# Performance work log

Hardware: AMD Instinct MI355X
Metric: run time of the kernel (lower is better)

## Reference

```python
import jax, jax.numpy as jnp
import numpy as np
import math

H = 8
D_MODEL = 512
D_K = D_MODEL // H
NEG = -1.0e9


def setup_inputs() -> dict:
    key = jax.random.key(0)
    ks = jax.random.split(key, 10)
    B, S, D = 8, 1024, D_MODEL
    s = 1.0 / math.sqrt(D)
    return {
        "query": jax.random.normal(ks[0], (B, S, D), jnp.float32),
        "key": jax.random.normal(ks[1], (B, S, D), jnp.float32),
        "value": jax.random.normal(ks[2], (B, S, D), jnp.float32),
        "group_prob": jax.random.uniform(ks[3], (B, S, S), jnp.float32),
        "Wq": jax.random.normal(ks[4], (D, D), jnp.float32) * s,
        "Wk": jax.random.normal(ks[5], (D, D), jnp.float32) * s,
        "Wv": jax.random.normal(ks[6], (D, D), jnp.float32) * s,
        "Wh": jax.random.normal(ks[7], (D, D), jnp.float32) * s,
        "bh": jax.random.normal(ks[8], (D,), jnp.float32) * s,
        "mask": jax.random.randint(ks[9], (B, S, S), 0, 2, jnp.int32),
    }


def reference(query, key, value, group_prob, Wq, Wk, Wv, Wh, bh, mask):
    B, S, D = query.shape
    # project and split heads: [B, H, S, d_k]
    def split(x, W):
        return (x @ W.T).reshape(B, S, H, D_K).transpose(0, 2, 1, 3)
    q, k, v = split(query, Wq), split(key, Wk), split(value, Wv)
    scores = jnp.einsum('bhqd,bhkd->bhqk', q, k) / jnp.sqrt(jnp.asarray(D_K, q.dtype))
    # masked_fill where (mask | eye) == 0, i.e. keep mask-allowed or diagonal positions
    eye = jnp.eye(S, dtype=jnp.int32)
    allowed = (mask[:, None, :, :] | eye[None, None, :, :]) != 0  # [B,1,S,S]
    scores = jnp.where(allowed, scores, jnp.asarray(NEG, scores.dtype))
    p_attn = jax.nn.softmax(scores, axis=-1)
    p_attn = p_attn * group_prob[:, None, :, :]  # post-softmax group scaling
    x = jnp.einsum('bhqk,bhkd->bhqd', p_attn, v)
    x = x.transpose(0, 2, 1, 3).reshape(B, S, D)
    return x @ Wh.T + bh
```

## Files before the change

kernel.cpp:

```cpp
#include <hip/hip_runtime.h>
#include <hip/hip_bf16.h>
#include <cstdint>


typedef __attribute__((ext_vector_type(8))) short short8;
typedef __attribute__((ext_vector_type(4))) float f32x4;

__device__ __forceinline__ ushort f2bf(float x) {
    union { __hip_bfloat16 h; ushort u; } v;
    v.h = __float2bfloat16(x);
    return v.u;
}
__device__ __forceinline__ float bf2f(ushort u) {
    union { uint u; float f; } v; v.u = ((uint)u) << 16; return v.f;
}
__device__ __forceinline__ f32x4 mfma16(short8 a, short8 b, f32x4 c) {
    return __builtin_amdgcn_mfma_f32_16x16x32_bf16(a, b, c, 0, 0, 0);
}

__global__ __launch_bounds__(256)
void gm_prep(const int* __restrict__ mask, const float* __restrict__ gp,
             ushort* __restrict__ gm)
{
    size_t i = ((size_t)blockIdx.x * 256 + threadIdx.x) * 4;
    int4 m = *(const int4*)(mask + i);
    float4 g = *(const float4*)(gp + i);
    int k = (int)(i & 1023), q = (int)((i >> 10) & 1023);
    const ushort neg = f2bf(-1.0f);
    ushort4 o;
    o.x = (m.x != 0 || q == k + 0) ? f2bf(g.x) : neg;
    o.y = (m.y != 0 || q == k + 1) ? f2bf(g.y) : neg;
    o.z = (m.z != 0 || q == k + 2) ? f2bf(g.z) : neg;
    o.w = (m.w != 0 || q == k + 3) ? f2bf(g.w) : neg;
    *(ushort4*)(gm + i) = o;
}

__global__ __launch_bounds__(256)
void qkv_gemm(const float* __restrict__ Xq, const float* __restrict__ Xk,
              const float* __restrict__ Xv,
              const float* __restrict__ Wq, const float* __restrict__ Wk,
              const float* __restrict__ Wv,
              ushort* __restrict__ q_ws, ushort* __restrict__ k_ws,
              ushort* __restrict__ vT)
{
    __shared__ __attribute__((aligned(16))) ushort As[128][40];
    __shared__ __attribute__((aligned(16))) ushort Bs[128][40];

    const int z = blockIdx.z;
    const float* A  = (z == 0) ? Xq : (z == 1) ? Xk : Wv;
    const float* Bm = (z == 0) ? Wq : (z == 1) ? Wk : Xv;
    const int mt = (z == 2) ? blockIdx.y : blockIdx.x;
    const int nt = (z == 2) ? blockIdx.x : blockIdx.y;
    const int m0 = mt * 128, n0 = nt * 128;
    const int tid = threadIdx.x;
    const int lane = tid & 63, wave = tid >> 6;
    const int l15 = lane & 15, g = lane >> 4;
    const int wm = wave >> 1, wn = wave & 1;
    const int srow = tid >> 1, skh = (tid & 1) * 16;

    f32x4 acc[4][4];
    #pragma unroll
    for (int i = 0; i < 4; ++i)
        #pragma unroll
        for (int j = 0; j < 4; ++j) acc[i][j] = (f32x4){0.f, 0.f, 0.f, 0.f};

    const float* Arow = A  + (size_t)(m0 + srow) * 512 + skh;
    const float* Brow = Bm + (size_t)(n0 + srow) * 512 + skh;

    for (int k0 = 0; k0 < 512; k0 += 32) {
        {
            float4 a0 = *(const float4*)(Arow + k0);
            float4 a1 = *(const float4*)(Arow + k0 + 4);
            float4 a2 = *(const float4*)(Arow + k0 + 8);
            float4 a3 = *(const float4*)(Arow + k0 + 12);
            short8 w0, w1;
            w0[0]=(short)f2bf(a0.x); w0[1]=(short)f2bf(a0.y); w0[2]=(short)f2bf(a0.z); w0[3]=(short)f2bf(a0.w);
            w0[4]=(short)f2bf(a1.x); w0[5]=(short)f2bf(a1.y); w0[6]=(short)f2bf(a1.z); w0[7]=(short)f2bf(a1.w);
            w1[0]=(short)f2bf(a2.x); w1[1]=(short)f2bf(a2.y); w1[2]=(short)f2bf(a2.z); w1[3]=(short)f2bf(a2.w);
            w1[4]=(short)f2bf(a3.x); w1[5]=(short)f2bf(a3.y); w1[6]=(short)f2bf(a3.z); w1[7]=(short)f2bf(a3.w);
            *(short8*)&As[srow][skh]     = w0;
            *(short8*)&As[srow][skh + 8] = w1;
            float4 b0 = *(const float4*)(Brow + k0);
            float4 b1 = *(const float4*)(Brow + k0 + 4);
            float4 b2 = *(const float4*)(Brow + k0 + 8);
            float4 b3 = *(const float4*)(Brow + k0 + 12);
            short8 u0, u1;
            u0[0]=(short)f2bf(b0.x); u0[1]=(short)f2bf(b0.y); u0[2]=(short)f2bf(b0.z); u0[3]=(short)f2bf(b0.w);
            u0[4]=(short)f2bf(b1.x); u0[5]=(short)f2bf(b1.y); u0[6]=(short)f2bf(b1.z); u0[7]=(short)f2bf(b1.w);
            u1[0]=(short)f2bf(b2.x); u1[1]=(short)f2bf(b2.y); u1[2]=(short)f2bf(b2.z); u1[3]=(short)f2bf(b2.w);
            u1[4]=(short)f2bf(b3.x); u1[5]=(short)f2bf(b3.y); u1[6]=(short)f2bf(b3.z); u1[7]=(short)f2bf(b3.w);
            *(short8*)&Bs[srow][skh]     = u0;
            *(short8*)&Bs[srow][skh + 8] = u1;
        }
        __syncthreads();
        short8 af[4], bfr[4];
        #pragma unroll
        for (int i = 0; i < 4; ++i)
            af[i] = *(const short8*)&As[wm * 64 + i * 16 + l15][g * 8];
        #pragma unroll
        for (int j = 0; j < 4; ++j)
            bfr[j] = *(const short8*)&Bs[wn * 64 + j * 16 + l15][g * 8];
        #pragma unroll
        for (int i = 0; i < 4; ++i)
            #pragma unroll
            for (int j = 0; j < 4; ++j)
                acc[i][j] = mfma16(af[i], bfr[j], acc[i][j]);
        __syncthreads();
    }

    #pragma unroll
    for (int i = 0; i < 4; ++i) {
        #pragma unroll
        for (int j = 0; j < 4; ++j) {
            #pragma unroll
            for (int r = 0; r < 4; ++r) {
                int mm = m0 + wm * 64 + i * 16 + g * 4 + r;
                int nn = n0 + wn * 64 + j * 16 + l15;
                float val = acc[i][j][r];
                if (z == 2) {
                    int h = mm >> 6, d = mm & 63, b = nn >> 10, s = nn & 1023;
                    vT[(((size_t)(b * 8 + h) * 64 + d) << 10) + s] = f2bf(val);
                } else {
                    int b = mm >> 10, s = mm & 1023, h = nn >> 6, dk = nn & 63;
                    ushort* dst = (z == 0) ? q_ws : k_ws;
                    dst[((((size_t)(b * 8 + h)) << 10) + s) * 64 + dk] = f2bf(val);
                }
            }
        }
    }
}

__global__ __launch_bounds__(256)
void out_gemm(const ushort* __restrict__ Xh, const float* __restrict__ Wh,
              const float* __restrict__ bias, float* __restrict__ out)
{
    __shared__ __attribute__((aligned(16))) ushort As[128][40];
    __shared__ __attribute__((aligned(16))) ushort Bs[128][40];

    const int m0 = blockIdx.x * 128, n0 = blockIdx.y * 128;
    const int tid = threadIdx.x;
    const int lane = tid & 63, wave = tid >> 6;
    const int l15 = lane & 15, g = lane >> 4;
    const int wm = wave >> 1, wn = wave & 1;
    const int srow = tid >> 1, skh = (tid & 1) * 16;

    f32x4 acc[4][4];
    #pragma unroll
    for (int i = 0; i < 4; ++i)
        #pragma unroll
        for (int j = 0; j < 4; ++j) acc[i][j] = (f32x4){0.f, 0.f, 0.f, 0.f};

    const int m = m0 + srow;
    const int b = m >> 10, s = m & 1023;
    const float* Brow = Wh + (size_t)(n0 + srow) * 512 + skh;

    for (int k0 = 0; k0 < 512; k0 += 32) {
        {
            int kk = k0 + skh;
            int h = kk >> 6, dd = kk & 63;
            const ushort* src = Xh + ((((size_t)(b * 8 + h)) << 10) + s) * 64 + dd;
            *(short8*)&As[srow][skh]     = *(const short8*)src;
            *(short8*)&As[srow][skh + 8] = *(const short8*)(src + 8);
            float4 b0 = *(const float4*)(Brow + k0);
            float4 b1 = *(const float4*)(Brow + k0 + 4);
            float4 b2 = *(const float4*)(Brow + k0 + 8);
            float4 b3 = *(const float4*)(Brow + k0 + 12);
            short8 u0, u1;
            u0[0]=(short)f2bf(b0.x); u0[1]=(short)f2bf(b0.y); u0[2]=(short)f2bf(b0.z); u0[3]=(short)f2bf(b0.w);
            u0[4]=(short)f2bf(b1.x); u0[5]=(short)f2bf(b1.y); u0[6]=(short)f2bf(b1.z); u0[7]=(short)f2bf(b1.w);
            u1[0]=(short)f2bf(b2.x); u1[1]=(short)f2bf(b2.y); u1[2]=(short)f2bf(b2.z); u1[3]=(short)f2bf(b2.w);
            u1[4]=(short)f2bf(b3.x); u1[5]=(short)f2bf(b3.y); u1[6]=(short)f2bf(b3.z); u1[7]=(short)f2bf(b3.w);
            *(short8*)&Bs[srow][skh]     = u0;
            *(short8*)&Bs[srow][skh + 8] = u1;
        }
        __syncthreads();
        short8 af[4], bfr[4];
        #pragma unroll
        for (int i = 0; i < 4; ++i)
            af[i] = *(const short8*)&As[wm * 64 + i * 16 + l15][g * 8];
        #pragma unroll
        for (int j = 0; j < 4; ++j)
            bfr[j] = *(const short8*)&Bs[wn * 64 + j * 16 + l15][g * 8];
        #pragma unroll
        for (int i = 0; i < 4; ++i)
            #pragma unroll
            for (int j = 0; j < 4; ++j)
                acc[i][j] = mfma16(af[i], bfr[j], acc[i][j]);
        __syncthreads();
    }

    float bv[4];
    #pragma unroll
    for (int j = 0; j < 4; ++j) bv[j] = bias[n0 + wn * 64 + j * 16 + l15];

    #pragma unroll
    for (int i = 0; i < 4; ++i) {
        #pragma unroll
        for (int j = 0; j < 4; ++j) {
            #pragma unroll
            for (int r = 0; r < 4; ++r) {
                int mm = m0 + wm * 64 + i * 16 + g * 4 + r;
                int nn = n0 + wn * 64 + j * 16 + l15;
                out[(size_t)mm * 512 + nn] = acc[i][j][r] + bv[j];
            }
        }
    }
}

__global__ __launch_bounds__(512, 2)
void attn(const ushort* __restrict__ Qh, const ushort* __restrict__ Kh,
          const ushort* __restrict__ Vt, const ushort* __restrict__ gm,
          ushort* __restrict__ xo)
{
    __shared__ __attribute__((aligned(16))) ushort kvbuf[2][2][4096];

    const int w = blockIdx.x;
    const int bh = w & 63, qt = w >> 6;
    const int tid = threadIdx.x;
    const int wave = tid >> 6, lane = tid & 63;
    const int l15 = lane & 15, g = lane >> 4;
    const int q0 = qt * 128 + wave * 16;
    const int b = bh >> 3;

    const ushort* Qp  = Qh + ((size_t)bh * 1024 + q0 + l15) * 64;
    const char*   Kpb = (const char*)(Kh + (size_t)bh * 65536);
    const char*   Vpb = (const char*)(Vt + (size_t)bh * 65536);
    const ushort* gmp = gm + ((size_t)b * 1024 + q0 + l15) * 1024;

    const short8 qf0 = *(const short8*)(Qp + g * 8);
    const short8 qf1 = *(const short8*)(Qp + 32 + g * 8);

    const int Xr  = wave * 1024 + lane * 16;
    const int r_k = Xr >> 7;
    const int cb  = Xr & 127;
    const int pp   = (r_k & 3) | (((r_k >> 3) & 3) << 2) |
                     (((r_k >> 2) & 1) << 4) | ((r_k >> 5) << 5);
    const int kdst = pp * 128 + (cb ^ ((pp & 7) << 4));
    const int vdst = r_k * 128 + (cb ^ ((r_k & 7) << 4));

    const int sw    = (l15 & 7) << 4;
    const int kcol0 = (g * 16) ^ sw;
    const int kcol1 = (64 + g * 16) ^ sw;

    f32x4 ot[4];
    #pragma unroll
    for (int t = 0; t < 4; ++t) ot[t] = (f32x4){0.f, 0.f, 0.f, 0.f};
    float m2 = -1.0e30f, lsum = 0.f;
    const float SC = 0.125f * 1.44269504f;

    uint4 kst = *(const uint4*)(Kpb + (size_t)r_k * 128 + cb);
    uint4 vst = *(const uint4*)(Vpb + (size_t)r_k * 2048 + cb);
    *(uint4*)((char*)&kvbuf[0][0][0] + kdst) = kst;
    *(uint4*)((char*)&kvbuf[0][1][0] + vdst) = vst;
    kst = *(const uint4*)(Kpb + (size_t)(64 + r_k) * 128 + cb);
    vst = *(const uint4*)(Vpb + (size_t)r_k * 2048 + 128 + cb);
    short8 gmc0 = *(const short8*)(gmp + g * 8);
    short8 gmc1 = *(const short8*)(gmp + 32 + g * 8);
    short8 gmn0 = *(const short8*)(gmp + 64 + g * 8);
    short8 gmn1 = *(const short8*)(gmp + 96 + g * 8);
    __syncthreads();

    for (int t = 0; t < 16; ++t) {
        const int cur = t & 1;
        if (t < 15) {
            *(uint4*)((char*)&kvbuf[cur ^ 1][0][0] + kdst) = kst;
            *(uint4*)((char*)&kvbuf[cur ^ 1][1][0] + vdst) = vst;
        }
        const char* kb = (const char*)&kvbuf[cur][0][0];
        const char* vb = (const char*)&kvbuf[cur][1][0];

        f32x4 s4[4];
        #pragma unroll
        for (int t4 = 0; t4 < 4; ++t4) {
            const char* ka = kb + (t4 * 16 + l15) * 128;
            short8 k0f = *(const short8*)(ka + kcol0);
            short8 k1f = *(const short8*)(ka + kcol1);
            f32x4 zz = (f32x4){0.f, 0.f, 0.f, 0.f};
            zz = mfma16(k0f, qf0, zz);
            zz = mfma16(k1f, qf1, zz);
            s4[t4] = zz;
        }

        float tmax = -1.0e30f;
        #pragma unroll
        for (int c = 0; c < 2; ++c) {
            const short8 gc = c ? gmc1 : gmc0;
            #pragma unroll
            for (int j = 0; j < 8; ++j) {
                float gv = bf2f((ushort)gc[j]);
                int t4 = 2 * c + (j >> 2), r = j & 3;
                float sv = s4[t4][r] * SC;
                sv = (gv >= 0.f) ? sv : -1.0e9f;
                s4[t4][r] = sv;
                tmax = fmaxf(tmax, sv);
            }
        }
        tmax = fmaxf(tmax, __shfl_xor(tmax, 16, 64));
        tmax = fmaxf(tmax, __shfl_xor(tmax, 32, 64));

        if (__any(tmax > m2 + 4.0f)) {
            float mnew = fmaxf(m2, tmax);
            float corr = exp2f(m2 - mnew);
            m2 = mnew;
            lsum *= corr;
            #pragma unroll
            for (int t4 = 0; t4 < 4; ++t4) {
                ot[t4][0] *= corr; ot[t4][1] *= corr;
                ot[t4][2] *= corr; ot[t4][3] *= corr;
            }
        }

        short8 pa0, pa1;
        #pragma unroll
        for (int c = 0; c < 2; ++c) {
            const short8 gc = c ? gmc1 : gmc0;
            #pragma unroll
            for (int j = 0; j < 8; ++j) {
                int t4 = 2 * c + (j >> 2), r = j & 3;
                float p = exp2f(s4[t4][r] - m2);
                lsum += p;
                float pg = p * bf2f((ushort)gc[j]);
                if (c) pa1[j] = (short)f2bf(pg); else pa0[j] = (short)f2bf(pg);
            }
        }

        #pragma unroll
        for (int td = 0; td < 4; ++td) {
            const char* va = vb + (td * 16 + l15) * 128;
            short8 v0 = *(const short8*)(va + kcol0);
            short8 v1 = *(const short8*)(va + kcol1);
            ot[td] = mfma16(v0, pa0, ot[td]);
            ot[td] = mfma16(v1, pa1, ot[td]);
        }

        if (t < 14) {
            const int k0n = (t + 2) * 64;
            kst = *(const uint4*)(Kpb + (size_t)(k0n + r_k) * 128 + cb);
            vst = *(const uint4*)(Vpb + (size_t)r_k * 2048 + (size_t)k0n * 2 + cb);
        }
        gmc0 = gmn0; gmc1 = gmn1;
        if (t < 14) {
            const int k0n = (t + 2) * 64;
            gmn0 = *(const short8*)(gmp + k0n + g * 8);
            gmn1 = *(const short8*)(gmp + k0n + 32 + g * 8);
        }
        __syncthreads();
    }

    lsum += __shfl_xor(lsum, 16, 64);
    lsum += __shfl_xor(lsum, 32, 64);
    const float inv = 1.0f / lsum;

    ushort* xp = xo + ((size_t)bh * 1024 + q0 + l15) * 64;
    #pragma unroll
    for (int td = 0; td < 4; ++td)
        #pragma unroll
        for (int r = 0; r < 4; ++r)
            xp[td * 16 + g * 4 + r] = f2bf(ot[td][r] * inv);
}

extern "C" void kernel_launch(void* const* d_in, const int* in_sizes, int n_in,
                              void* d_out, int out_size, void* d_ws, size_t ws_size,
                              hipStream_t stream)
{
    const float* query = (const float*)d_in[0];
    const float* key   = (const float*)d_in[1];
    const float* value = (const float*)d_in[2];
    const float* gprob = (const float*)d_in[3];
    const float* Wq    = (const float*)d_in[4];
    const float* Wk    = (const float*)d_in[5];
    const float* Wv    = (const float*)d_in[6];
    const float* Wh    = (const float*)d_in[7];
    const float* bh    = (const float*)d_in[8];
    const int*   mask  = (const int*)d_in[9];
    float* out = (float*)d_out;

    ushort* ws = (ushort*)d_ws;
    const size_t HS = (size_t)64 * 65536;
    ushort* q_ws = ws;
    ushort* k_ws = ws + HS;
    ushort* vT   = ws + 2 * HS;
    ushort* x_ws = ws + 3 * HS;
    ushort* gmb  = ws + 4 * HS;

    qkv_gemm<<<dim3(64, 4, 3), 256, 0, stream>>>(query, key, value, Wq, Wk, Wv,
                                                 q_ws, k_ws, vT);
    gm_prep<<<8192, 256, 0, stream>>>(mask, gprob, gmb);
    attn<<<512, 512, 0, stream>>>(q_ws, k_ws, vT, gmb, x_ws);
    out_gemm<<<dim3(64, 4), 256, 0, stream>>>(x_ws, Wh, bh, out);
}
```

Baseline: 110.0 us.

## Pre-convert inputs to bf16, use direct global-to-LDS loads with swizzled tiles

```diff
diff --git a/kernel.cpp b/kernel.cpp
--- a/kernel.cpp
+++ b/kernel.cpp
@@ -14,49 +14,101 @@
 __device__ __forceinline__ float bf2f(ushort u) {
     union { uint u; float f; } v; v.u = ((uint)u) << 16; return v.f;
 }
+__device__ __forceinline__ uint cvtpk(float lo, float hi) {
+    uint r;
+    asm("v_cvt_pk_bf16_f32 %0, %1, %2" : "=v"(r) : "v"(lo), "v"(hi));
+    return r;
+}
 __device__ __forceinline__ f32x4 mfma16(short8 a, short8 b, f32x4 c) {
     return __builtin_amdgcn_mfma_f32_16x16x32_bf16(a, b, c, 0, 0, 0);
 }
+__device__ __forceinline__ void gl16(const void* g, const void* l) {
+    __builtin_amdgcn_global_load_lds(
+        (const __attribute__((address_space(1))) uint32_t*)(uintptr_t)g,
+        (__attribute__((address_space(3))) uint32_t*)(uint32_t)(uintptr_t)l,
+        16, 0, 0);
+}
 
 __global__ __launch_bounds__(256)
-void gm_prep(const int* __restrict__ mask, const float* __restrict__ gp,
-             ushort* __restrict__ gm)
+void prep(const float* __restrict__ q, const float* __restrict__ k,
+          const float* __restrict__ v,
+          const float* __restrict__ wq, const float* __restrict__ wk,
+          const float* __restrict__ wv, const float* __restrict__ wh,
+          const int* __restrict__ mask, const float* __restrict__ gp,
+          ushort* __restrict__ qb, ushort* __restrict__ kb,
+          ushort* __restrict__ vb,
+          ushort* __restrict__ wqb, ushort* __restrict__ wkb,
+          ushort* __restrict__ wvb, ushort* __restrict__ whb,
+          ushort* __restrict__ gmb)
 {
-    size_t i = ((size_t)blockIdx.x * 256 + threadIdx.x) * 4;
-    int4 m = *(const int4*)(mask + i);
-    float4 g = *(const float4*)(gp + i);
-    int k = (int)(i & 1023), q = (int)((i >> 10) & 1023);
-    const ushort neg = f2bf(-1.0f);
-    ushort4 o;
-    o.x = (m.x != 0 || q == k + 0) ? f2bf(g.x) : neg;
-    o.y = (m.y != 0 || q == k + 1) ? f2bf(g.y) : neg;
-    o.z = (m.z != 0 || q == k + 2) ? f2bf(g.z) : neg;
-    o.w = (m.w != 0 || q == k + 3) ? f2bf(g.w) : neg;
-    *(ushort4*)(gm + i) = o;
-}
-
-__global__ __launch_bounds__(256)
-void qkv_gemm(const float* __restrict__ Xq, const float* __restrict__ Xk,
-              const float* __restrict__ Xv,
-              const float* __restrict__ Wq, const float* __restrict__ Wk,
-              const float* __restrict__ Wv,
-              ushort* __restrict__ q_ws, ushort* __restrict__ k_ws,
-              ushort* __restrict__ vT)
+    const int bid = blockIdx.x, tid = threadIdx.x;
+    if (bid < 8192) {
+        size_t i = ((size_t)bid * 256 + tid) * 4;
+        int4 m = *(const int4*)(mask + i);
+        float4 gg = *(const float4*)(gp + i);
+        int kk = (int)(i & 1023), qq = (int)((i >> 10) & 1023);
+        uint u01 = cvtpk(gg.x, gg.y), u23 = cvtpk(gg.z, gg.w);
+        ushort4 o;
+        o.x = (m.x != 0 || qq == kk + 0) ? (ushort)(u01 & 0xffff) : (ushort)0xBF80;
+        o.y = (m.y != 0 || qq == kk + 1) ? (ushort)(u01 >> 16)    : (ushort)0xBF80;
+        o.z = (m.z != 0 || qq == kk + 2) ? (ushort)(u23 & 0xffff) : (ushort)0xBF80;
+        o.w = (m.w != 0 || qq == kk + 3) ? (ushort)(u23 >> 16)    : (ushort)0xBF80;
+        *(ushort4*)(gmb + i) = o;
+    } else if (bid < 20480) {
+        size_t id = ((size_t)(bid - 8192) * 256 + tid) * 4;
+        int t = (int)(id >> 22);
+        size_t off = id & 4194303;
+        const float* s = (t == 0) ? q : (t == 1) ? k : v;
+        ushort* d = (t == 0) ? qb : (t == 1) ? kb : vb;
+        float4 x = *(const float4*)(s + off);
+        uint2 o; o.x = cvtpk(x.x, x.y); o.y = cvtpk(x.z, x.w);
+        *(uint2*)(d + off) = o;
+    } else {
+        size_t id = ((size_t)(bid - 20480) * 256 + tid) * 4;
+        int t = (int)(id >> 18);
+        size_t off = id & 262143;
+        const float* s = (t == 0) ? wq : (t == 1) ? wk : (t == 2) ? wv : wh;
+        ushort* d = (t == 0) ? wqb : (t == 1) ? wkb : (t == 2) ? wvb : whb;
+        float4 x = *(const float4*)(s + off);
+        uint2 o; o.x = cvtpk(x.x, x.y); o.y = cvtpk(x.z, x.w);
+        *(uint2*)(d + off) = o;
+    }
+}
+
+__global__ __launch_bounds__(256, 2)
+void gemm3(const ushort* __restrict__ qb, const ushort* __restrict__ kb,
+           const ushort* __restrict__ vb,
+           const ushort* __restrict__ Wqb, const ushort* __restrict__ Wkb,
+           const ushort* __restrict__ Wvb,
+           ushort* __restrict__ q_ws, ushort* __restrict__ k_ws,
+           ushort* __restrict__ vT)
 {
-    __shared__ __attribute__((aligned(16))) ushort As[128][40];
-    __shared__ __attribute__((aligned(16))) ushort Bs[128][40];
+    __shared__ __attribute__((aligned(16))) ushort As[8192];
+    __shared__ __attribute__((aligned(16))) ushort Bs[8192];
 
     const int z = blockIdx.z;
-    const float* A  = (z == 0) ? Xq : (z == 1) ? Xk : Wv;
-    const float* Bm = (z == 0) ? Wq : (z == 1) ? Wk : Xv;
+    const ushort* A = (z == 0) ? qb : (z == 1) ? kb : Wvb;
+    const ushort* B = (z == 0) ? Wqb : (z == 1) ? Wkb : vb;
     const int mt = (z == 2) ? blockIdx.y : blockIdx.x;
     const int nt = (z == 2) ? blockIdx.x : blockIdx.y;
     const int m0 = mt * 128, n0 = nt * 128;
-    const int tid = threadIdx.x;
-    const int lane = tid & 63, wave = tid >> 6;
+    const int tid = threadIdx.x, lane = tid & 63, wave = tid >> 6;
     const int l15 = lane & 15, g = lane >> 4;
     const int wm = wave >> 1, wn = wave & 1;
-    const int srow = tid >> 1, skh = (tid & 1) * 16;
+
+    const int cb = (lane & 7) << 4;
+    int soff[4];
+    #pragma unroll
+    for (int it = 0; it < 4; ++it) {
+        int r = (it * 4 + wave) * 8 + (lane >> 3);
+        soff[it] = r * 1024 + (cb ^ ((r & 7) << 4));
+    }
+    const char* Ab = (const char*)A + (size_t)m0 * 1024;
+    const char* Bb = (const char*)B + (size_t)n0 * 1024;
+
+    const int sw = (l15 & 7) << 4;
+    const int c0 = (g * 16) ^ sw;
+    const int c1 = (64 + g * 16) ^ sw;
 
     f32x4 acc[4][4];
     #pragma unroll
@@ -64,47 +116,30 @@
         #pragma unroll
         for (int j = 0; j < 4; ++j) acc[i][j] = (f32x4){0.f, 0.f, 0.f, 0.f};
 
-    const float* Arow = A  + (size_t)(m0 + srow) * 512 + skh;
-    const float* Brow = Bm + (size_t)(n0 + srow) * 512 + skh;
-
-    for (int k0 = 0; k0 < 512; k0 += 32) {
-        {
-            float4 a0 = *(const float4*)(Arow + k0);
-            float4 a1 = *(const float4*)(Arow + k0 + 4);
-            float4 a2 = *(const float4*)(Arow + k0 + 8);
-            float4 a3 = *(const float4*)(Arow + k0 + 12);
-            short8 w0, w1;
-            w0[0]=(short)f2bf(a0.x); w0[1]=(short)f2bf(a0.y); w0[2]=(short)f2bf(a0.z); w0[3]=(short)f2bf(a0.w);
-            w0[4]=(short)f2bf(a1.x); w0[5]=(short)f2bf(a1.y); w0[6]=(short)f2bf(a1.z); w0[7]=(short)f2bf(a1.w);
-            w1[0]=(short)f2bf(a2.x); w1[1]=(short)f2bf(a2.y); w1[2]=(short)f2bf(a2.z); w1[3]=(short)f2bf(a2.w);
-            w1[4]=(short)f2bf(a3.x); w1[5]=(short)f2bf(a3.y); w1[6]=(short)f2bf(a3.z); w1[7]=(short)f2bf(a3.w);
-            *(short8*)&As[srow][skh]     = w0;
-            *(short8*)&As[srow][skh + 8] = w1;
-            float4 b0 = *(const float4*)(Brow + k0);
-            float4 b1 = *(const float4*)(Brow + k0 + 4);
-            float4 b2 = *(const float4*)(Brow + k0 + 8);
-            float4 b3 = *(const float4*)(Brow + k0 + 12);
-            short8 u0, u1;
-            u0[0]=(short)f2bf(b0.x); u0[1]=(short)f2bf(b0.y); u0[2]=(short)f2bf(b0.z); u0[3]=(short)f2bf(b0.w);
-            u0[4]=(short)f2bf(b1.x); u0[5]=(short)f2bf(b1.y); u0[6]=(short)f2bf(b1.z); u0[7]=(short)f2bf(b1.w);
-            u1[0]=(short)f2bf(b2.x); u1[1]=(short)f2bf(b2.y); u1[2]=(short)f2bf(b2.z); u1[3]=(short)f2bf(b2.w);
-            u1[4]=(short)f2bf(b3.x); u1[5]=(short)f2bf(b3.y); u1[6]=(short)f2bf(b3.z); u1[7]=(short)f2bf(b3.w);
-            *(short8*)&Bs[srow][skh]     = u0;
-            *(short8*)&Bs[srow][skh + 8] = u1;
+    for (int ks = 0; ks < 8; ++ks) {
+        const int kof = ks * 128;
+        #pragma unroll
+        for (int it = 0; it < 4; ++it) {
+            gl16(Ab + soff[it] + kof, (const char*)As + (it * 4 + wave) * 1024);
+            gl16(Bb + soff[it] + kof, (const char*)Bs + (it * 4 + wave) * 1024);
         }
         __syncthreads();
-        short8 af[4], bfr[4];
-        #pragma unroll
-        for (int i = 0; i < 4; ++i)
-            af[i] = *(const short8*)&As[wm * 64 + i * 16 + l15][g * 8];
-        #pragma unroll
-        for (int j = 0; j < 4; ++j)
-            bfr[j] = *(const short8*)&Bs[wn * 64 + j * 16 + l15][g * 8];
-        #pragma unroll
-        for (int i = 0; i < 4; ++i)
+        #pragma unroll
+        for (int kk = 0; kk < 2; ++kk) {
+            const int cc = kk ? c1 : c0;
+            short8 af[4], bf[4];
+            #pragma unroll
+            for (int i = 0; i < 4; ++i)
+                af[i] = *(const short8*)((const char*)As + (wm * 64 + i * 16 + l15) * 128 + cc);
             #pragma unroll
             for (int j = 0; j < 4; ++j)
-                acc[i][j] = mfma16(af[i], bfr[j], acc[i][j]);
+                bf[j] = *(const short8*)((const char*)Bs + (wn * 64 + j * 16 + l15) * 128 + cc);
+            #pragma unroll
+            for (int i = 0; i < 4; ++i)
+                #pragma unroll
+                for (int j = 0; j < 4; ++j)
+                    acc[i][j] = mfma16(af[i], bf[j], acc[i][j]);
+        }
         __syncthreads();
     }
 
@@ -117,32 +152,47 @@
                 int mm = m0 + wm * 64 + i * 16 + g * 4 + r;
                 int nn = n0 + wn * 64 + j * 16 + l15;
                 float val = acc[i][j][r];
-                if (z == 2) {
+                if (z == 0) {
+                    val *= 0.18033688f;
+                    int b = mm >> 10, s = mm & 1023, h = nn >> 6, dk = nn & 63;
+                    q_ws[((((size_t)(b * 8 + h)) << 10) + s) * 64 + dk] = f2bf(val);
+                } else if (z == 1) {
+                    int b = mm >> 10, s = mm & 1023, h = nn >> 6, dk = nn & 63;
+                    k_ws[((((size_t)(b * 8 + h)) << 10) + s) * 64 + dk] = f2bf(val);
+                } else {
                     int h = mm >> 6, d = mm & 63, b = nn >> 10, s = nn & 1023;
                     vT[(((size_t)(b * 8 + h) * 64 + d) << 10) + s] = f2bf(val);
-                } else {
-                    int b = mm >> 10, s = mm & 1023, h = nn >> 6, dk = nn & 63;
-                    ushort* dst = (z == 0) ? q_ws : k_ws;
-                    dst[((((size_t)(b * 8 + h)) << 10) + s) * 64 + dk] = f2bf(val);
                 }
             }
         }
     }
 }
 
-__global__ __launch_bounds__(256)
-void out_gemm(const ushort* __restrict__ Xh, const float* __restrict__ Wh,
-              const float* __restrict__ bias, float* __restrict__ out)
+__global__ __launch_bounds__(256, 2)
+void gemm_o(const ushort* __restrict__ Xh, const ushort* __restrict__ Whb,
+            const float* __restrict__ bias, float* __restrict__ out)
 {
-    __shared__ __attribute__((aligned(16))) ushort As[128][40];
-    __shared__ __attribute__((aligned(16))) ushort Bs[128][40];
+    __shared__ __attribute__((aligned(16))) ushort As[8192];
+    __shared__ __attribute__((aligned(16))) ushort Bs[8192];
 
     const int m0 = blockIdx.x * 128, n0 = blockIdx.y * 128;
-    const int tid = threadIdx.x;
-    const int lane = tid & 63, wave = tid >> 6;
+    const int tid = threadIdx.x, lane = tid & 63, wave = tid >> 6;
     const int l15 = lane & 15, g = lane >> 4;
     const int wm = wave >> 1, wn = wave & 1;
-    const int srow = tid >> 1, skh = (tid & 1) * 16;
+    const int bb = m0 >> 10, s0 = m0 & 1023;
+
+    const int cb = (lane & 7) << 4;
+    int aoff[4], boff[4];
+    #pragma unroll
+    for (int it = 0; it < 4; ++it) {
+        int r = (it * 4 + wave) * 8 + (lane >> 3);
+        int swz = cb ^ ((r & 7) << 4);
+        aoff[it] = ((bb * 8) * 1024 + s0 + r) * 128 + swz;
+        boff[it] = (n0 + r) * 1024 + swz;
+    }
+    const int sw = (l15 & 7) << 4;
+    const int c0 = (g * 16) ^ sw;
+    const int c1 = (64 + g * 16) ^ sw;
 
     f32x4 acc[4][4];
     #pragma unroll
@@ -150,159 +200,152 @@
         #pragma unroll
         for (int j = 0; j < 4; ++j) acc[i][j] = (f32x4){0.f, 0.f, 0.f, 0.f};
 
-    const int m = m0 + srow;
-    const int b = m >> 10, s = m & 1023;
-    const float* Brow = Wh + (size_t)(n0 + srow) * 512 + skh;
-
-    for (int k0 = 0; k0 < 512; k0 += 32) {
-        {
-            int kk = k0 + skh;
-            int h = kk >> 6, dd = kk & 63;
-            const ushort* src = Xh + ((((size_t)(b * 8 + h)) << 10) + s) * 64 + dd;
-            *(short8*)&As[srow][skh]     = *(const short8*)src;
-            *(short8*)&As[srow][skh + 8] = *(const short8*)(src + 8);
-            float4 b0 = *(const float4*)(Brow + k0);
-            float4 b1 = *(const float4*)(Brow + k0 + 4);
-            float4 b2 = *(const float4*)(Brow + k0 + 8);
-            float4 b3 = *(const float4*)(Brow + k0 + 12);
-            short8 u0, u1;
-            u0[0]=(short)f2bf(b0.x); u0[1]=(short)f2bf(b0.y); u0[2]=(short)f2bf(b0.z); u0[3]=(short)f2bf(b0.w);
-            u0[4]=(short)f2bf(b1.x); u0[5]=(short)f2bf(b1.y); u0[6]=(short)f2bf(b1.z); u0[7]=(short)f2bf(b1.w);
-            u1[0]=(short)f2bf(b2.x); u1[1]=(short)f2bf(b2.y); u1[2]=(short)f2bf(b2.z); u1[3]=(short)f2bf(b2.w);
-            u1[4]=(short)f2bf(b3.x); u1[5]=(short)f2bf(b3.y); u1[6]=(short)f2bf(b3.z); u1[7]=(short)f2bf(b3.w);
-            *(short8*)&Bs[srow][skh]     = u0;
-            *(short8*)&Bs[srow][skh + 8] = u1;
+    for (int ks = 0; ks < 8; ++ks) {
+        #pragma unroll
+        for (int it = 0; it < 4; ++it) {
+            gl16((const char*)Xh + aoff[it] + ks * 131072,
+                 (const char*)As + (it * 4 + wave) * 1024);
+            gl16((const char*)Whb + boff[it] + ks * 128,
+                 (const char*)Bs + (it * 4 + wave) * 1024);
         }
         __syncthreads();
-        short8 af[4], bfr[4];
-        #pragma unroll
-        for (int i = 0; i < 4; ++i)
-            af[i] = *(const short8*)&As[wm * 64 + i * 16 + l15][g * 8];
+        #pragma unroll
+        for (int kk = 0; kk < 2; ++kk) {
+            const int cc = kk ? c1 : c0;
+            short8 af[4], bf[4];
+            #pragma unroll
+            for (int i = 0; i < 4; ++i)
+                af[i] = *(const short8*)((const char*)As + (wm * 64 + i * 16 + l15) * 128 + cc);
+            #pragma unroll
+            for (int j = 0; j < 4; ++j)
+                bf[j] = *(const short8*)((const char*)Bs + (wn * 64 + j * 16 + l15) * 128 + cc);
+            #pragma unroll
+            for (int i = 0; i < 4; ++i)
+                #pragma unroll
+                for (int j = 0; j < 4; ++j)
+                    acc[i][j] = mfma16(af[i], bf[j], acc[i][j]);
+        }
+        __syncthreads();
+    }
+
+    float bv[4];
+    #pragma unroll
+    for (int j = 0; j < 4; ++j) bv[j] = bias[n0 + wn * 64 + j * 16 + l15];
+
+    #pragma unroll
+    for (int i = 0; i < 4; ++i)
         #pragma unroll
         for (int j = 0; j < 4; ++j)
-            bfr[j] = *(const short8*)&Bs[wn * 64 + j * 16 + l15][g * 8];
-        #pragma unroll
-        for (int i = 0; i < 4; ++i)
-            #pragma unroll
-            for (int j = 0; j < 4; ++j)
-                acc[i][j] = mfma16(af[i], bfr[j], acc[i][j]);
-        __syncthreads();
-    }
-
-    float bv[4];
-    #pragma unroll
-    for (int j = 0; j < 4; ++j) bv[j] = bias[n0 + wn * 64 + j * 16 + l15];
-
-    #pragma unroll
-    for (int i = 0; i < 4; ++i) {
-        #pragma unroll
-        for (int j = 0; j < 4; ++j) {
             #pragma unroll
             for (int r = 0; r < 4; ++r) {
                 int mm = m0 + wm * 64 + i * 16 + g * 4 + r;
                 int nn = n0 + wn * 64 + j * 16 + l15;
                 out[(size_t)mm * 512 + nn] = acc[i][j][r] + bv[j];
             }
-        }
-    }
-}
-
-__global__ __launch_bounds__(512, 2)
+}
+
+__global__ __launch_bounds__(256, 4)
 void attn(const ushort* __restrict__ Qh, const ushort* __restrict__ Kh,
           const ushort* __restrict__ Vt, const ushort* __restrict__ gm,
           ushort* __restrict__ xo)
 {
-    __shared__ __attribute__((aligned(16))) ushort kvbuf[2][2][4096];
+    __shared__ __attribute__((aligned(16))) ushort kv[2][2][4096];
 
     const int w = blockIdx.x;
     const int bh = w & 63, qt = w >> 6;
-    const int tid = threadIdx.x;
-    const int wave = tid >> 6, lane = tid & 63;
+    const int tid = threadIdx.x, wave = tid >> 6, lane = tid & 63;
     const int l15 = lane & 15, g = lane >> 4;
-    const int q0 = qt * 128 + wave * 16;
+    const int q0 = qt * 64 + wave * 16;
     const int b = bh >> 3;
 
-    const ushort* Qp  = Qh + ((size_t)bh * 1024 + q0 + l15) * 64;
-    const char*   Kpb = (const char*)(Kh + (size_t)bh * 65536);
-    const char*   Vpb = (const char*)(Vt + (size_t)bh * 65536);
+    const char* Kpb = (const char*)(Kh + (size_t)bh * 65536);
+    const char* Vpb = (const char*)(Vt + (size_t)bh * 65536);
+    const ushort* Qp = Qh + ((size_t)bh * 1024 + q0 + l15) * 64;
     const ushort* gmp = gm + ((size_t)b * 1024 + q0 + l15) * 1024;
 
     const short8 qf0 = *(const short8*)(Qp + g * 8);
     const short8 qf1 = *(const short8*)(Qp + 32 + g * 8);
 
-    const int Xr  = wave * 1024 + lane * 16;
-    const int r_k = Xr >> 7;
-    const int cb  = Xr & 127;
-    const int pp   = (r_k & 3) | (((r_k >> 3) & 3) << 2) |
-                     (((r_k >> 2) & 1) << 4) | ((r_k >> 5) << 5);
-    const int kdst = pp * 128 + (cb ^ ((pp & 7) << 4));
-    const int vdst = r_k * 128 + (cb ^ ((r_k & 7) << 4));
-
-    const int sw    = (l15 & 7) << 4;
-    const int kcol0 = (g * 16) ^ sw;
-    const int kcol1 = (64 + g * 16) ^ sw;
+    const int cb = (lane & 7) << 4;
+    const int rA = wave * 8 + (lane >> 3);
+    const int rB = rA + 32;
+    const int gkA = (rA & 3) + 4 * ((rA >> 4) & 1) + 8 * ((rA >> 2) & 3) + 32 * (rA >> 5);
+    const int gkB = (rB & 3) + 4 * ((rB >> 4) & 1) + 8 * ((rB >> 2) & 3) + 32 * (rB >> 5);
+    const int okA = gkA * 128 + (cb ^ ((rA & 7) << 4));
+    const int okB = gkB * 128 + (cb ^ ((rB & 7) << 4));
+    const int ovA = rA * 2048 + (cb ^ ((rA & 7) << 4));
+    const int ovB = rB * 2048 + (cb ^ ((rB & 7) << 4));
+
+    const int sw = (l15 & 7) << 4;
+    const int c0 = (g * 16) ^ sw;
+    const int c1 = (64 + g * 16) ^ sw;
 
     f32x4 ot[4];
     #pragma unroll
     for (int t = 0; t < 4; ++t) ot[t] = (f32x4){0.f, 0.f, 0.f, 0.f};
     float m2 = -1.0e30f, lsum = 0.f;
-    const float SC = 0.125f * 1.44269504f;
-
-    uint4 kst = *(const uint4*)(Kpb + (size_t)r_k * 128 + cb);
-    uint4 vst = *(const uint4*)(Vpb + (size_t)r_k * 2048 + cb);
-    *(uint4*)((char*)&kvbuf[0][0][0] + kdst) = kst;
-    *(uint4*)((char*)&kvbuf[0][1][0] + vdst) = vst;
-    kst = *(const uint4*)(Kpb + (size_t)(64 + r_k) * 128 + cb);
-    vst = *(const uint4*)(Vpb + (size_t)r_k * 2048 + 128 + cb);
+
+    gl16(Kpb + okA, &kv[0][0][wave * 512]);
+    gl16(Kpb + okB, &kv[0][0][(4 + wave) * 512]);
+    gl16(Vpb + ovA, &kv[0][1][wave * 512]);
+    gl16(Vpb + ovB, &kv[0][1][(4 + wave) * 512]);
     short8 gmc0 = *(const short8*)(gmp + g * 8);
     short8 gmc1 = *(const short8*)(gmp + 32 + g * 8);
-    short8 gmn0 = *(const short8*)(gmp + 64 + g * 8);
-    short8 gmn1 = *(const short8*)(gmp + 96 + g * 8);
     __syncthreads();
 
     for (int t = 0; t < 16; ++t) {
         const int cur = t & 1;
+        short8 gmn0, gmn1;
         if (t < 15) {
-            *(uint4*)((char*)&kvbuf[cur ^ 1][0][0] + kdst) = kst;
-            *(uint4*)((char*)&kvbuf[cur ^ 1][1][0] + vdst) = vst;
-        }
-        const char* kb = (const char*)&kvbuf[cur][0][0];
-        const char* vb = (const char*)&kvbuf[cur][1][0];
+            const char* kp = Kpb + (size_t)(t + 1) * 8192;
+            const char* vp = Vpb + (size_t)(t + 1) * 128;
+            gl16(kp + okA, &kv[cur ^ 1][0][wave * 512]);
+            gl16(kp + okB, &kv[cur ^ 1][0][(4 + wave) * 512]);
+            gl16(vp + ovA, &kv[cur ^ 1][1][wave * 512]);
+            gl16(vp + ovB, &kv[cur ^ 1][1][(4 + wave) * 512]);
+            gmn0 = *(const short8*)(gmp + (t + 1) * 64 + g * 8);
+            gmn1 = *(const short8*)(gmp + (t + 1) * 64 + 32 + g * 8);
+        }
+        const char* kbuf = (const char*)&kv[cur][0][0];
+        const char* vbuf = (const char*)&kv[cur][1][0];
 
         f32x4 s4[4];
         #pragma unroll
         for (int t4 = 0; t4 < 4; ++t4) {
-            const char* ka = kb + (t4 * 16 + l15) * 128;
-            short8 k0f = *(const short8*)(ka + kcol0);
-            short8 k1f = *(const short8*)(ka + kcol1);
+            const char* ka = kbuf + (t4 * 16 + l15) * 128;
+            short8 k0f = *(const short8*)(ka + c0);
+            short8 k1f = *(const short8*)(ka + c1);
             f32x4 zz = (f32x4){0.f, 0.f, 0.f, 0.f};
             zz = mfma16(k0f, qf0, zz);
             zz = mfma16(k1f, qf1, zz);
             s4[t4] = zz;
         }
 
-        float tmax = -1.0e30f;
+        float gv[16], svv[16];
         #pragma unroll
         for (int c = 0; c < 2; ++c) {
             const short8 gc = c ? gmc1 : gmc0;
             #pragma unroll
             for (int j = 0; j < 8; ++j) {
-                float gv = bf2f((ushort)gc[j]);
-                int t4 = 2 * c + (j >> 2), r = j & 3;
-                float sv = s4[t4][r] * SC;
-                sv = (gv >= 0.f) ? sv : -1.0e9f;
-                s4[t4][r] = sv;
-                tmax = fmaxf(tmax, sv);
+                const int jj = c * 8 + j;
+                const int t4 = 2 * c + (j >> 2), r = j & 3;
+                float gvv = bf2f((ushort)gc[j]);
+                gv[jj] = gvv;
+                svv[jj] = (gvv >= 0.f) ? s4[t4][r] : -1.0e9f;
             }
         }
+        float x0 = fmaxf(fmaxf(svv[0], svv[1]), fmaxf(svv[2], svv[3]));
+        float x1 = fmaxf(fmaxf(svv[4], svv[5]), fmaxf(svv[6], svv[7]));
+        float x2 = fmaxf(fmaxf(svv[8], svv[9]), fmaxf(svv[10], svv[11]));
+        float x3 = fmaxf(fmaxf(svv[12], svv[13]), fmaxf(svv[14], svv[15]));
+        float tmax = fmaxf(fmaxf(x0, x1), fmaxf(x2, x3));
         tmax = fmaxf(tmax, __shfl_xor(tmax, 16, 64));
         tmax = fmaxf(tmax, __shfl_xor(tmax, 32, 64));
 
         if (__any(tmax > m2 + 4.0f)) {
             float mnew = fmaxf(m2, tmax);
             float corr = exp2f(m2 - mnew);
-            m2 = mnew;
-            lsum *= corr;
+            m2 = mnew; lsum *= corr;
             #pragma unroll
             for (int t4 = 0; t4 < 4; ++t4) {
                 ot[t4][0] *= corr; ot[t4][1] *= corr;
@@ -310,41 +353,31 @@
             }
         }
 
-        short8 pa0, pa1;
-        #pragma unroll
-        for (int c = 0; c < 2; ++c) {
-            const short8 gc = c ? gmc1 : gmc0;
-            #pragma unroll
-            for (int j = 0; j < 8; ++j) {
-                int t4 = 2 * c + (j >> 2), r = j & 3;
-                float p = exp2f(s4[t4][r] - m2);
-                lsum += p;
-                float pg = p * bf2f((ushort)gc[j]);
-                if (c) pa1[j] = (short)f2bf(pg); else pa0[j] = (short)f2bf(pg);
-            }
-        }
+        float p[16];
+        #pragma unroll
+        for (int jj = 0; jj < 16; ++jj) p[jj] = exp2f(svv[jj] - m2);
+        lsum += (((p[0] + p[1]) + (p[2] + p[3])) + ((p[4] + p[5]) + (p[6] + p[7])))
+              + (((p[8] + p[9]) + (p[10] + p[11])) + ((p[12] + p[13]) + (p[14] + p[15])));
+        union { uint4 u; short8 s; } pa0, pa1;
+        pa0.u.x = cvtpk(p[0] * gv[0],  p[1] * gv[1]);
+        pa0.u.y = cvtpk(p[2] * gv[2],  p[3] * gv[3]);
+        pa0.u.z = cvtpk(p[4] * gv[4],  p[5] * gv[5]);
+        pa0.u.w = cvtpk(p[6] * gv[6],  p[7] * gv[7]);
+        pa1.u.x = cvtpk(p[8] * gv[8],  p[9] * gv[9]);
+        pa1.u.y = cvtpk(p[10] * gv[10], p[11] * gv[11]);
+        pa1.u.z = cvtpk(p[12] * gv[12], p[13] * gv[13]);
+        pa1.u.w = cvtpk(p[14] * gv[14], p[15] * gv[15]);
 
         #pragma unroll
         for (int td = 0; td < 4; ++td) {
-            const char* va = vb + (td * 16 + l15) * 128;
-            short8 v0 = *(const short8*)(va + kcol0);
-            short8 v1 = *(const short8*)(va + kcol1);
-            ot[td] = mfma16(v0, pa0, ot[td]);
-            ot[td] = mfma16(v1, pa1, ot[td]);
-        }
-
-        if (t < 14) {
-            const int k0n = (t + 2) * 64;
-            kst = *(const uint4*)(Kpb + (size_t)(k0n + r_k) * 128 + cb);
-            vst = *(const uint4*)(Vpb + (size_t)r_k * 2048 + (size_t)k0n * 2 + cb);
-        }
-        gmc0 = gmn0; gmc1 = gmn1;
-        if (t < 14) {
-            const int k0n = (t + 2) * 64;
-            gmn0 = *(const short8*)(gmp + k0n + g * 8);
-            gmn1 = *(const short8*)(gmp + k0n + 32 + g * 8);
+            const char* va = vbuf + (td * 16 + l15) * 128;
+            short8 v0 = *(const short8*)(va + c0);
+            short8 v1 = *(const short8*)(va + c1);
+            ot[td] = mfma16(v0, pa0.s, ot[td]);
+            ot[td] = mfma16(v1, pa1.s, ot[td]);
         }
         __syncthreads();
+        if (t < 15) { gmc0 = gmn0; gmc1 = gmn1; }
     }
 
     lsum += __shfl_xor(lsum, 16, 64);
@@ -353,10 +386,12 @@
 
     ushort* xp = xo + ((size_t)bh * 1024 + q0 + l15) * 64;
     #pragma unroll
-    for (int td = 0; td < 4; ++td)
-        #pragma unroll
-        for (int r = 0; r < 4; ++r)
-            xp[td * 16 + g * 4 + r] = f2bf(ot[td][r] * inv);
+    for (int td = 0; td < 4; ++td) {
+        uint2 o;
+        o.x = cvtpk(ot[td][0] * inv, ot[td][1] * inv);
+        o.y = cvtpk(ot[td][2] * inv, ot[td][3] * inv);
+        *(uint2*)(xp + td * 16 + g * 4) = o;
+    }
 }
 
 extern "C" void kernel_launch(void* const* d_in, const int* in_sizes, int n_in,
@@ -380,12 +415,21 @@
     ushort* q_ws = ws;
     ushort* k_ws = ws + HS;
     ushort* vT   = ws + 2 * HS;
-    ushort* x_ws = ws + 3 * HS;
-    ushort* gmb  = ws + 4 * HS;
-
-    qkv_gemm<<<dim3(64, 4, 3), 256, 0, stream>>>(query, key, value, Wq, Wk, Wv,
-                                                 q_ws, k_ws, vT);
-    gm_prep<<<8192, 256, 0, stream>>>(mask, gprob, gmb);
-    attn<<<512, 512, 0, stream>>>(q_ws, k_ws, vT, gmb, x_ws);
-    out_gemm<<<dim3(64, 4), 256, 0, stream>>>(x_ws, Wh, bh, out);
-}
+    ushort* gmb  = ws + 3 * HS;
+    ushort* qb   = ws + 5 * HS;
+    ushort* kb   = ws + 6 * HS;
+    ushort* vb   = ws + 7 * HS;
+    ushort* wqb  = ws + 8 * HS;
+    ushort* wkb  = wqb + 262144;
+    ushort* wvb  = wkb + 262144;
+    ushort* whb  = wvb + 262144;
+    ushort* x_ws = qb;
+
+    prep<<<21504, 256, 0, stream>>>(query, key, value, Wq, Wk, Wv, Wh,
+                                    mask, gprob, qb, kb, vb,
+                                    wqb, wkb, wvb, whb, gmb);
+    gemm3<<<dim3(64, 4, 3), 256, 0, stream>>>(qb, kb, vb, wqb, wkb, wvb,
+                                              q_ws, k_ws, vT);
+    attn<<<1024, 256, 0, stream>>>(q_ws, k_ws, vT, gmb, x_ws);
+    gemm_o<<<dim3(64, 4), 256, 0, stream>>>(x_ws, whb, bh, out);
+}
```

New measurement: 102.3 us. -7.1%, faster.
